# Kernel tuning notes

Hardware: AMD Instinct MI355X
Metric: run time of the kernel (lower is better)

Reference implementation:

```python
import jax, jax.numpy as jnp
import numpy as np

EPS = 1e-7
LN_EPS = 1e-6


def project(x):
    norm = jnp.maximum(jnp.linalg.norm(x, axis=-1, keepdims=True), EPS)
    max_norm = 1.0 - EPS
    return jnp.where(norm >= 1.0, x / norm * max_norm, x)


def mobius_add(x, y, c):
    x2 = jnp.sum(x * x, -1, keepdims=True)
    y2 = jnp.sum(y * y, -1, keepdims=True)
    xy = jnp.sum(x * y, -1, keepdims=True)
    num = (1 + 2 * c * xy + c * y2) * x + (1 - c * x2) * y
    den = 1 + 2 * c * xy + c * c * x2 * y2
    return project(num / jnp.maximum(den, EPS))


def logmap0(y, c):
    sqrt_c = jnp.maximum(jnp.sqrt(c), EPS)
    y_norm = jnp.linalg.norm(y, axis=-1, keepdims=True)
    safe = jnp.maximum(y_norm, EPS)
    mag = jnp.arctanh(jnp.minimum(y_norm, 1.0 - EPS)) / sqrt_c
    return jnp.where(y_norm < EPS, jnp.zeros_like(y), mag * (y / safe))


def expmap0(v, c):
    sqrt_c = jnp.maximum(jnp.sqrt(c), EPS)
    v_norm = jnp.linalg.norm(v, axis=-1, keepdims=True)
    safe = jnp.maximum(v_norm, EPS)
    mag = jnp.tanh(sqrt_c * safe) / sqrt_c
    return project(jnp.where(v_norm < EPS, jnp.zeros_like(v), mag * (v / safe)))


def poincare_dist(x, y, c):
    # x: [B,H,N,1,D], y: [B,H,N,W,D], c: [B,1,1,1,1] -> dist [B,H,N,W]
    sqrt_c = jnp.maximum(jnp.sqrt(c), EPS)
    add_norm = jnp.linalg.norm(mobius_add(-x, y, c), axis=-1)
    arg = jnp.minimum(sqrt_c.squeeze(-1) * add_norm, 1.0 - EPS)
    return 2.0 * jnp.arctanh(arg) / sqrt_c.squeeze(-1)


def sliding_windows(x, window):
    # x: [B,H,N,Dh] -> [B,H,N,window,Dh] of the last `window` keys per query (zero-padded)
    B, H, N, Dh = x.shape
    pad = jnp.zeros((B, H, window - 1, Dh), dtype=x.dtype)
    xp = jnp.concatenate([pad, x], axis=2)
    idx = jnp.arange(window)[None, :] + jnp.arange(N)[:, None]  # [N, W]
    return xp[:, :, idx, :]


def layer_norm(x, scale, bias):
    mu = jnp.mean(x, axis=-1, keepdims=True)
    var = jnp.mean(jnp.square(x - mu), axis=-1, keepdims=True)
    return (x - mu) * jax.lax.rsqrt(var + LN_EPS) * scale + bias


def setup_inputs() -> dict:
    key = jax.random.key(0)
    B, N, DIM, H = 2, 1024, 1024, 16
    Dh = DIM // H
    ks = jax.random.split(key, 16)
    s = 1.0 / np.sqrt(DIM)
    x = 0.01 * jax.random.normal(ks[0], (B, N, DIM), jnp.float32)  # well inside the ball
    # rotary angles: pos * inv_freq, shape [N, Dh//2]
    inv_freq = 1.0 / (10000.0 ** (np.arange(0, Dh // 2, dtype=np.float32) * 2.0 / Dh))
    freqs = jnp.asarray(np.arange(N, dtype=np.float32)[:, None] * inv_freq[None, :])
    c = 0.5 + 0.5 * jax.random.uniform(ks[1], (B,), jnp.float32)
    p = {
        'Wq': s * jax.random.normal(ks[2], (DIM, DIM), jnp.float32), 'bq': jnp.zeros((DIM,), jnp.float32),
        'Wk': s * jax.random.normal(ks[3], (DIM, DIM), jnp.float32), 'bk': jnp.zeros((DIM,), jnp.float32),
        'Wv': s * jax.random.normal(ks[4], (DIM, DIM), jnp.float32), 'bv': jnp.zeros((DIM,), jnp.float32),
        'Wo': s * jax.random.normal(ks[5], (DIM, DIM), jnp.float32), 'bo': jnp.zeros((DIM,), jnp.float32),
        'W1': s * jax.random.normal(ks[6], (DIM, 4 * DIM), jnp.float32), 'b1': jnp.zeros((4 * DIM,), jnp.float32),
        'W2': (1.0 / np.sqrt(4 * DIM)) * jax.random.normal(ks[7], (4 * DIM, DIM), jnp.float32), 'b2': jnp.zeros((DIM,), jnp.float32),
        'ln1_scale': jnp.ones((DIM,), jnp.float32), 'ln1_bias': jnp.zeros((DIM,), jnp.float32),
        'ln2_scale': jnp.ones((DIM,), jnp.float32), 'ln2_bias': jnp.zeros((DIM,), jnp.float32),
        'geo_scale': jnp.ones((H, 1, 1), jnp.float32),
    }
    return dict(x=x, freqs=freqs, c=c, **p)


def reference(x, freqs, c, Wq, bq, Wk, bk, Wv, bv, Wo, bo, W1, b1, W2, b2,
              ln1_scale, ln1_bias, ln2_scale, ln2_bias, geo_scale):
    WINDOW = 32
    B, N, DIM = x.shape
    H = geo_scale.shape[0]
    Dh = DIM // H
    c_ln = c.reshape(B, 1, 1)
    c_attn = c.reshape(B, 1, 1, 1)
    c_d = c.reshape(B, 1, 1, 1, 1)

    # tangent-space layer norm 1
    x_norm = expmap0(layer_norm(logmap0(x, c_ln), ln1_scale, ln1_bias), c_ln)
    x_tan = logmap0(x_norm, c_ln)

    q = (x_tan @ Wq + bq).reshape(B, N, H, Dh)
    k = (x_tan @ Wk + bk).reshape(B, N, H, Dh)
    v = (x_tan @ Wv + bv).reshape(B, N, H, Dh)

    # rotary embedding (real-arithmetic form of complex multiply)
    cos = jnp.cos(freqs).reshape(1, N, 1, Dh // 2)
    sin = jnp.sin(freqs).reshape(1, N, 1, Dh // 2)

    def rope(t):
        t_r, t_i = jnp.split(t, 2, -1)
        return jnp.concatenate([t_r * cos - t_i * sin, t_r * sin + t_i * cos], -1)

    q_hyp = expmap0(rope(q), c_attn)
    k_hyp = expmap0(rope(k), c_attn)

    q_t = q_hyp.transpose(0, 2, 1, 3)  # [B,H,N,Dh]
    k_t = k_hyp.transpose(0, 2, 1, 3)
    v_t = v.transpose(0, 2, 1, 3)

    k_w = sliding_windows(k_t, WINDOW)  # [B,H,N,W,Dh]
    v_w = sliding_windows(v_t, WINDOW)

    dist = poincare_dist(q_t[:, :, :, None, :], k_w, c_d)  # [B,H,N,W]
    attn = jax.nn.softmax(-geo_scale * dist, axis=-1)
    attn_out = jnp.einsum('bhnw,bhnwd->bhnd', attn, v_w).transpose(0, 2, 1, 3).reshape(B, N, DIM)

    attn_hyp = expmap0(attn_out @ Wo + bo, c_ln)
    x_att = mobius_add(x, attn_hyp, c_ln)

    # tangent-space layer norm 2 + hyperbolic FFN
    x_norm2 = expmap0(layer_norm(logmap0(x_att, c_ln), ln2_scale, ln2_bias), c_ln)
    t = logmap0(x_norm2, c_ln)
    ffn_tan = jax.nn.gelu(t @ W1 + b1) @ W2 + b2
    x_ffn = expmap0(ffn_tan, c_ln)
    return mobius_add(x_att, x_ffn, c_ln)
```

## Files before the change

kernel.cpp:

```cpp
#include <hip/hip_runtime.h>
#include <cmath>

static constexpr int SEQ = 1024;
static constexpr int DIM = 1024;
static constexpr int NH  = 16;
static constexpr int DH  = 64;
static constexpr int WB  = 2;
static constexpr int ROWS = WB * SEQ;
__device__ static constexpr double D_EPS = 1e-7;

typedef unsigned short ushort_t;
typedef __attribute__((ext_vector_type(8))) short short8v;
typedef __attribute__((ext_vector_type(4))) float float4v;

__device__ __forceinline__ uint32_t bf16_hi_bits(float f) {
  uint32_t u = __float_as_uint(f);
  return (u + 0x7fffu + ((u >> 16) & 1u)) >> 16;
}

__device__ __forceinline__ size_t tiled_addr(int row, int col, int Kld) {
  return ((size_t)(row >> 7) * (Kld >> 5) + (col >> 5)) * 4096
       + (size_t)((((row >> 4) & 7) << 9) + (((col >> 3) & 3) << 7) + ((row & 15) << 3) + (col & 7));
}
__device__ __forceinline__ void store_hl(ushort_t* __restrict__ hi, ushort_t* __restrict__ lo,
                                         size_t addr, float f) {
  const uint32_t hb = bf16_hi_bits(f);
  hi[addr] = (ushort_t)hb;
  lo[addr] = (ushort_t)bf16_hi_bits(f - __uint_as_float(hb << 16));
}

__device__ __forceinline__ double wsum64(double v) {
#pragma unroll
  for (int m = 32; m >= 1; m >>= 1) v += __shfl_xor(v, m, 64);
  return v;
}

__global__ __launch_bounds__(256) void conv_w_kernel(
    const float* __restrict__ W, ushort_t* __restrict__ hi, ushort_t* __restrict__ lo,
    int K, int N) {
  const int tid = blockIdx.x * 256 + threadIdx.x;
  const int n = tid % N;
  const int k0 = (tid / N) << 3;
  uint32_t hw[4], lw[4];
#pragma unroll
  for (int rp = 0; rp < 4; rp++) {
    uint32_t h2[2], l2[2];
#pragma unroll
    for (int e = 0; e < 2; e++) {
      const float f = W[(size_t)(k0 + rp * 2 + e) * N + n];
      const uint32_t hb = bf16_hi_bits(f);
      h2[e] = hb;
      l2[e] = bf16_hi_bits(f - __uint_as_float(hb << 16));
    }
    hw[rp] = h2[0] | (h2[1] << 16);
    lw[rp] = l2[0] | (l2[1] << 16);
  }
  const size_t addr = tiled_addr(n, k0, K);
  *(uint4*)&hi[addr] = *(uint4*)hw;
  *(uint4*)&lo[addr] = *(uint4*)lw;
}

__global__ __launch_bounds__(256) void ln_tan_kernel(
    const float* __restrict__ xin, const float* __restrict__ cb,
    const float* __restrict__ gamma, const float* __restrict__ beta,
    ushort_t* __restrict__ ohi, ushort_t* __restrict__ olo) {
  __shared__ double sh[2][4];
  const int row = blockIdx.x;
  const int b = row / SEQ;
  const float* xr = xin + (size_t)row * DIM;
  const int t = threadIdx.x;
  float xv[4];
  double s0 = 0.0, s1 = 0.0;
#pragma unroll
  for (int i = 0; i < 4; i++) {
    xv[i] = xr[t + 256 * i];
    s0 += (double)xv[i];
    s1 += (double)xv[i] * (double)xv[i];
  }
  s0 = wsum64(s0); s1 = wsum64(s1);
  const int wid = t >> 6, lane = t & 63;
  if (lane == 0) { sh[0][wid] = s0; sh[1][wid] = s1; }
  __syncthreads();
  s0 = sh[0][0] + sh[0][1] + sh[0][2] + sh[0][3];
  s1 = sh[1][0] + sh[1][1] + sh[1][2] + sh[1][3];

  const double cc  = (double)cb[b];
  const double sqc = fmax(sqrt(cc), D_EPS);
  const double xn  = sqrt(s1);
  double a = 0.0;
  if (xn >= D_EPS) a = atanh(fmin(xn, 1.0 - D_EPS)) / sqc / fmax(xn, D_EPS);
  const double mu   = a * s0 / (double)DIM;
  const double var  = a * a * s1 / (double)DIM - mu * mu;
  const double invs = 1.0 / sqrt(var + 1e-6);

  double tv[4]; double s2 = 0.0;
#pragma unroll
  for (int i = 0; i < 4; i++) {
    const int col = t + 256 * i;
    tv[i] = (a * (double)xv[i] - mu) * invs * (double)gamma[col] + (double)beta[col];
    s2 += tv[i] * tv[i];
  }
  s2 = wsum64(s2);
  __syncthreads();
  if (lane == 0) sh[0][wid] = s2;
  __syncthreads();
  s2 = sh[0][0] + sh[0][1] + sh[0][2] + sh[0][3];

  const double tn = sqrt(s2);
  double C = 0.0;
  if (tn >= D_EPS) {
    const double safe_t = fmax(tn, D_EPS);
    const double mag2 = tanh(sqc * safe_t) / sqc;
    const double en = mag2 * (tn / safe_t);
    const double pn = fmax(en, D_EPS);
    const double f  = (pn >= 1.0) ? (1.0 - D_EPS) / pn : 1.0;
    const double yn = en * f;
    if (yn >= D_EPS) {
      const double mag3 = atanh(fmin(yn, 1.0 - D_EPS)) / sqc;
      C = (mag2 / safe_t) * f * (mag3 / fmax(yn, D_EPS));
    }
  }
#pragma unroll
  for (int i = 0; i < 4; i++) {
    const int col = t + 256 * i;
    store_hl(ohi, olo, tiled_addr(row, col, DIM), (float)(tv[i] * C));
  }
}

__global__ __launch_bounds__(256) void expmobius_parts4_kernel(
    const float* __restrict__ xb,
    const float* __restrict__ p0, const float* __restrict__ p1,
    const float* __restrict__ p2, const float* __restrict__ p3,
    const float* __restrict__ bias, const float* __restrict__ cb,
    float* __restrict__ out) {
  __shared__ double sh[3][4];
  const int row = blockIdx.x;
  const int b = row / SEQ;
  const size_t ro = (size_t)row * DIM;
  const int t = threadIdx.x;
  float xv[4];
  double tv[4];
  double sx2 = 0.0, st2 = 0.0, sxt = 0.0;
#pragma unroll
  for (int i = 0; i < 4; i++) {
    const int col = t + 256 * i;
    xv[i] = xb[ro + col];
    tv[i] = (double)p0[ro + col] + (double)p1[ro + col] +
            (double)p2[ro + col] + (double)p3[ro + col] + (double)bias[col];
    sx2 += (double)xv[i] * (double)xv[i];
    st2 += tv[i] * tv[i];
    sxt += (double)xv[i] * tv[i];
  }
  sx2 = wsum64(sx2); st2 = wsum64(st2); sxt = wsum64(sxt);
  const int wid = t >> 6, lane = t & 63;
  if (lane == 0) { sh[0][wid] = sx2; sh[1][wid] = st2; sh[2][wid] = sxt; }
  __syncthreads();
  sx2 = sh[0][0] + sh[0][1] + sh[0][2] + sh[0][3];
  st2 = sh[1][0] + sh[1][1] + sh[1][2] + sh[1][3];
  sxt = sh[2][0] + sh[2][1] + sh[2][2] + sh[2][3];

  const double cc  = (double)cb[b];
  const double sqc = fmax(sqrt(cc), D_EPS);
  const double tn = sqrt(st2);
  double s = 0.0;
  if (tn >= D_EPS) {
    const double safe = fmax(tn, D_EPS);
    const double mag = tanh(sqc * safe) / sqc;
    const double en = mag * (tn / safe);
    const double pn = fmax(en, D_EPS);
    const double f  = (pn >= 1.0) ? (1.0 - D_EPS) / pn : 1.0;
    s = (mag / safe) * f;
  }
  const double x2 = sx2, y2 = s * s * st2, xy = s * sxt;
  const double P   = 1.0 + 2.0 * cc * xy + cc * y2;
  const double Q   = 1.0 - cc * x2;
  const double den = fmax(1.0 + 2.0 * cc * xy + cc * cc * x2 * y2, D_EPS);
  const double num2 = P * P * x2 + Q * Q * y2 + 2.0 * P * Q * xy;
  const double rn  = sqrt(fmax(num2, 0.0)) / den;
  const double pn2 = fmax(rn, D_EPS);
  const double pf  = (pn2 >= 1.0) ? (1.0 - D_EPS) / pn2 : 1.0;
  const double Pd = (P / den) * pf;
  const double Qd = (Q / den) * pf * s;
#pragma unroll
  for (int i = 0; i < 4; i++)
    out[ro + t + 256 * i] = (float)(Pd * (double)xv[i] + Qd * tv[i]);
}

__global__ __launch_bounds__(256) void rope_expmap_kernel(
    float* __restrict__ q, float* __restrict__ k,
    const float* __restrict__ freqs, const float* __restrict__ cb) {
  const int row = blockIdx.x;
  const int b = row / SEQ, n = row % SEQ;
  const int t = threadIdx.x;
  const int h = t >> 4, j = t & 15;
  const int p1 = j, p2 = j + 16;
  const double f1 = (double)freqs[n * (DH / 2) + p1];
  const double f2 = (double)freqs[n * (DH / 2) + p2];
  const double c1 = cos(f1), s1 = sin(f1);
  const double c2 = cos(f2), s2 = sin(f2);
  const double cc  = (double)cb[b];
  const double sqc = fmax(sqrt(cc), D_EPS);
  const size_t base = (size_t)row * DIM + (size_t)h * DH;
  float* arrs[2] = {q, k};
#pragma unroll
  for (int a = 0; a < 2; a++) {
    float* p = arrs[a] + base;
    const double xr1 = p[p1], xi1 = p[p1 + 32];
    const double xr2 = p[p2], xi2 = p[p2 + 32];
    const double r1 = xr1 * c1 - xi1 * s1, i1 = xr1 * s1 + xi1 * c1;
    const double r2 = xr2 * c2 - xi2 * s2, i2 = xr2 * s2 + xi2 * c2;
    double nrm2 = r1 * r1 + i1 * i1 + r2 * r2 + i2 * i2;
#pragma unroll
    for (int m = 8; m >= 1; m >>= 1) nrm2 += __shfl_xor(nrm2, m, 16);
    const double vn = sqrt(nrm2);
    double sc = 0.0;
    if (vn >= D_EPS) {
      const double safe = fmax(vn, D_EPS);
      const double mag = tanh(sqc * safe) / sqc;
      const double en = mag * (vn / safe);
      const double pn = fmax(en, D_EPS);
      const double f  = (pn >= 1.0) ? (1.0 - D_EPS) / pn : 1.0;
      sc = (mag / safe) * f;
    }
    p[p1] = (float)(r1 * sc); p[p1 + 32] = (float)(i1 * sc);
    p[p2] = (float)(r2 * sc); p[p2 + 32] = (float)(i2 * sc);
  }
}

__global__ __launch_bounds__(256) void attn_kernel(
    const float* __restrict__ qh, const float* __restrict__ kh,
    const float* __restrict__ v, const float* __restrict__ cb,
    const float* __restrict__ geo,
    ushort_t* __restrict__ ohi, ushort_t* __restrict__ olo) {
  __shared__ float qs[8][DH];
  const int g = threadIdx.x >> 5;
  const int w = threadIdx.x & 31;
  const int gid = blockIdx.x * 8 + g;
  const int n = gid & (SEQ - 1);
  const int bh = gid >> 10;
  const int h = bh & (NH - 1);
  const int b = bh >> 4;
  const int row = b * SEQ + n;
  const size_t qbase = (size_t)row * DIM + (size_t)h * DH;
  qs[g][w] = qh[qbase + w];
  qs[g][w + 32] = qh[qbase + w + 32];
  __syncthreads();

  const double cc  = (double)cb[b];
  const double sqc = fmax(sqrt(cc), D_EPS);
  double q2p = (double)qs[g][w] * qs[g][w] + (double)qs[g][w + 32] * qs[g][w + 32];
#pragma unroll
  for (int m = 16; m >= 1; m >>= 1) q2p += __shfl_xor(q2p, m, 32);
  const double a2 = q2p;

  const int msrc = n - 31 + w;
  double y2 = 0.0, qy = 0.0;
  if (msrc >= 0) {
    const float* kr = kh + ((size_t)(b * SEQ + msrc)) * DIM + (size_t)h * DH;
#pragma unroll 8
    for (int d = 0; d < DH; d++) {
      const double kv = (double)kr[d];
      y2 += kv * kv;
      qy += (double)qs[g][d] * kv;
    }
  }
  const double ay = -qy;
  const double P = 1.0 + 2.0 * cc * ay + cc * y2;
  const double Q = 1.0 - cc * a2;
  const double den = fmax(1.0 + 2.0 * cc * ay + cc * cc * a2 * y2, D_EPS);
  const double num2 = P * P * a2 + Q * Q * y2 + 2.0 * P * Q * ay;
  const double rn = sqrt(fmax(num2, 0.0)) / den;
  const double pn = fmax(rn, D_EPS);
  const double addn = (pn >= 1.0) ? (1.0 - D_EPS) * (rn / pn) : rn;
  const double arg = fmin(sqc * addn, 1.0 - D_EPS);
  const double dist = 2.0 * atanh(arg) / sqc;
  const double logit = -(double)geo[h] * dist;

  double mx = logit;
#pragma unroll
  for (int m = 16; m >= 1; m >>= 1) mx = fmax(mx, __shfl_xor(mx, m, 32));
  const double e = exp(logit - mx);
  double se = e;
#pragma unroll
  for (int m = 16; m >= 1; m >>= 1) se += __shfl_xor(se, m, 32);
  const double p = e / se;

  double acc1 = 0.0, acc2 = 0.0;
  for (int wp = 0; wp < 32; wp++) {
    const double pw = __shfl(p, wp, 32);
    const int mp = n - 31 + wp;
    if (mp >= 0) {
      const float* vr = v + ((size_t)(b * SEQ + mp)) * DIM + (size_t)h * DH;
      acc1 += pw * (double)vr[w];
      acc2 += pw * (double)vr[w + 32];
    }
  }
  const int col = h * DH + w;
  store_hl(ohi, olo, tiled_addr(row, col, DIM), (float)acc1);
  store_hl(ohi, olo, tiled_addr(row, col + 32, DIM), (float)acc2);
}

__device__ __forceinline__ float gelu_tanh(float x) {
  const float x3 = x * x * x;
  return 0.5f * x * (1.0f + tanhf(0.7978845608028654f * (x + 0.044715f * x3)));
}

template <int EPI>
__device__ __forceinline__ void mfma_gemm_body(
    const ushort_t* __restrict__ Ahi, const ushort_t* __restrict__ Alo, int Kld,
    const ushort_t* __restrict__ Bhi, const ushort_t* __restrict__ Blo, int KB,
    const float* __restrict__ bias, float* __restrict__ Cf,
    ushort_t* __restrict__ Chi, ushort_t* __restrict__ Clo, int KldOut,
    int N, int k0, int klen, int m0, int n0) {
  __shared__ __align__(16) short AsH[4096], AsL[4096], BsH[4096], BsL[4096];
  const int t = threadIdx.x;
  const int lane = t & 63, wave = t >> 6;
  const int wm = (wave >> 1) << 6, wn = (wave & 1) << 6;
  const size_t abase = (size_t)(m0 >> 7) * (Kld >> 5) * 4096;
  const size_t bbase = (size_t)(n0 >> 7) * (KB >> 5) * 4096;

  float4v acc[4][4];
#pragma unroll
  for (int i = 0; i < 4; i++)
#pragma unroll
    for (int j = 0; j < 4; j++) acc[i][j] = (float4v){0.f, 0.f, 0.f, 0.f};

  uint4 rah0, rah1, ral0, ral1, rbh0, rbh1, rbl0, rbl1;
  {
    const size_t at = abase + (size_t)(k0 >> 5) * 4096;
    const size_t bt = bbase + (size_t)(k0 >> 5) * 4096;
    rah0 = ((const uint4*)(Ahi + at))[t]; rah1 = ((const uint4*)(Ahi + at))[t + 256];
    ral0 = ((const uint4*)(Alo + at))[t]; ral1 = ((const uint4*)(Alo + at))[t + 256];
    rbh0 = ((const uint4*)(Bhi + bt))[t]; rbh1 = ((const uint4*)(Bhi + bt))[t + 256];
    rbl0 = ((const uint4*)(Blo + bt))[t]; rbl1 = ((const uint4*)(Blo + bt))[t + 256];
  }

  for (int kt = 0; kt < klen; kt += 32) {
    __syncthreads();
    ((uint4*)AsH)[t] = rah0; ((uint4*)AsH)[t + 256] = rah1;
    ((uint4*)AsL)[t] = ral0; ((uint4*)AsL)[t + 256] = ral1;
    ((uint4*)BsH)[t] = rbh0; ((uint4*)BsH)[t + 256] = rbh1;
    ((uint4*)BsL)[t] = rbl0; ((uint4*)BsL)[t + 256] = rbl1;
    __syncthreads();
    {
      const int ktn = (kt + 32 < klen) ? kt + 32 : kt;
      const size_t at = abase + (size_t)((k0 + ktn) >> 5) * 4096;
      const size_t bt = bbase + (size_t)((k0 + ktn) >> 5) * 4096;
      rah0 = ((const uint4*)(Ahi + at))[t]; rah1 = ((const uint4*)(Ahi + at))[t + 256];
      ral0 = ((const uint4*)(Alo + at))[t]; ral1 = ((const uint4*)(Alo + at))[t + 256];
      rbh0 = ((const uint4*)(Bhi + bt))[t]; rbh1 = ((const uint4*)(Bhi + bt))[t + 256];
      rbl0 = ((const uint4*)(Blo + bt))[t]; rbl1 = ((const uint4*)(Blo + bt))[t + 256];
    }
    short8v aH[4], aL[4];
    const int ams = wm >> 4;
#pragma unroll
    for (int im = 0; im < 4; im++) {
      aH[im] = *(const short8v*)&AsH[(((ams + im) << 6) + lane) << 3];
      aL[im] = *(const short8v*)&AsL[(((ams + im) << 6) + lane) << 3];
    }
    const int bns = wn >> 4;
#pragma unroll
    for (int in_ = 0; in_ < 4; in_++) {
      const short8v bH = *(const short8v*)&BsH[(((bns + in_) << 6) + lane) << 3];
      const short8v bL = *(const short8v*)&BsL[(((bns + in_) << 6) + lane) << 3];
#pragma unroll
      for (int im = 0; im < 4; im++) {
        acc[im][in_] = __builtin_amdgcn_mfma_f32_16x16x32_bf16(aH[im], bH, acc[im][in_], 0, 0, 0);
        acc[im][in_] = __builtin_amdgcn_mfma_f32_16x16x32_bf16(aH[im], bL, acc[im][in_], 0, 0, 0);
        acc[im][in_] = __builtin_amdgcn_mfma_f32_16x16x32_bf16(aL[im], bH, acc[im][in_], 0, 0, 0);
      }
    }
  }
  const int cq = lane >> 4, ci = lane & 15;
#pragma unroll
  for (int im = 0; im < 4; im++) {
    const int row = m0 + wm + im * 16 + cq * 4;
#pragma unroll
    for (int in_ = 0; in_ < 4; in_++) {
      const int col = n0 + wn + in_ * 16 + ci;
      if (EPI == 2) {
#pragma unroll
        for (int r = 0; r < 4; r++) Cf[(size_t)(row + r) * N + col] = acc[im][in_][r];
      } else if (EPI == 0) {
        const float bv_ = bias[col];
#pragma unroll
        for (int r = 0; r < 4; r++) Cf[(size_t)(row + r) * N + col] = acc[im][in_][r] + bv_;
      } else {
        const float bv_ = bias[col];
#pragma unroll
        for (int r = 0; r < 4; r++)
          store_hl(Chi, Clo, tiled_addr(row + r, col, KldOut),
                   gelu_tanh(acc[im][in_][r] + bv_));
      }
    }
  }
}

__global__ __launch_bounds__(256) void qkv_mfma(
    const ushort_t* __restrict__ Ahi, const ushort_t* __restrict__ Alo,
    const ushort_t* __restrict__ Whi, const ushort_t* __restrict__ Wlo,
    const float* __restrict__ bq, const float* __restrict__ bk, const float* __restrict__ bv,
    float* __restrict__ Cq, float* __restrict__ Ck, float* __restrict__ Cv) {
  const int which = blockIdx.x >> 3;
  const int n0 = (blockIdx.x & 7) << 7;
  const size_t woff = (size_t)which * (1u << 20);
  const float* bias = (which == 0) ? bq : (which == 1) ? bk : bv;
  float* C = (which == 0) ? Cq : (which == 1) ? Ck : Cv;
  mfma_gemm_body<0>(Ahi, Alo, DIM, Whi + woff, Wlo + woff, DIM, bias, C,
                    nullptr, nullptr, 0, DIM, 0, DIM, blockIdx.y << 7, n0);
}

__global__ __launch_bounds__(256) void ffn_up_mfma(
    const ushort_t* __restrict__ Ahi, const ushort_t* __restrict__ Alo,
    const ushort_t* __restrict__ W1hi, const ushort_t* __restrict__ W1lo,
    const float* __restrict__ b1, ushort_t* __restrict__ Hhi, ushort_t* __restrict__ Hlo) {
  mfma_gemm_body<1>(Ahi, Alo, DIM, W1hi, W1lo, DIM, b1, nullptr, Hhi, Hlo, 4 * DIM,
                    4 * DIM, 0, DIM, blockIdx.y << 7, blockIdx.x << 7);
}

__global__ __launch_bounds__(256) void gemm_splitk_mfma(
    const ushort_t* __restrict__ Ahi, const ushort_t* __restrict__ Alo, int Kld,
    const ushort_t* __restrict__ Bhi, const ushort_t* __restrict__ Blo, int KB,
    float* __restrict__ C0, float* __restrict__ C1,
    float* __restrict__ C2, float* __restrict__ C3, int N, int klen) {
  const int z = blockIdx.z;
  float* C = (z == 0) ? C0 : (z == 1) ? C1 : (z == 2) ? C2 : C3;
  mfma_gemm_body<2>(Ahi, Alo, Kld, Bhi, Blo, KB, nullptr, C, nullptr, nullptr, 0,
                    N, z * klen, klen, blockIdx.y << 7, blockIdx.x << 7);
}

extern "C" void kernel_launch(void* const* d_in, const int* in_sizes, int n_in,
                              void* d_out, int out_size, void* d_ws, size_t ws_size,
                              hipStream_t stream) {
  const float* x     = (const float*)d_in[0];
  const float* freqs = (const float*)d_in[1];
  const float* c     = (const float*)d_in[2];
  const float* Wq = (const float*)d_in[3];  const float* bq = (const float*)d_in[4];
  const float* Wk = (const float*)d_in[5];  const float* bk = (const float*)d_in[6];
  const float* Wv = (const float*)d_in[7];  const float* bv = (const float*)d_in[8];
  const float* Wo = (const float*)d_in[9];  const float* bo = (const float*)d_in[10];
  const float* W1 = (const float*)d_in[11]; const float* b1 = (const float*)d_in[12];
  const float* W2 = (const float*)d_in[13]; const float* b2 = (const float*)d_in[14];
  const float* g1 = (const float*)d_in[15]; const float* be1 = (const float*)d_in[16];
  const float* g2 = (const float*)d_in[17]; const float* be2 = (const float*)d_in[18];
  const float* geo = (const float*)d_in[19];
  float* out = (float*)d_out;
  float* ws = (float*)d_ws;

  const size_t SZ = (size_t)ROWS * DIM;
  const size_t PL = SZ;
  const uint32_t M1 = 1u << 20;
  auto us = [&](int i) { return (ushort_t*)(ws + (size_t)i * SZ); };

  ushort_t* xt_hi = us(0);           ushort_t* xt_lo = us(0) + PL;
  float* qb = ws + 1 * SZ; float* kb = ws + 2 * SZ; float* vb = ws + 3 * SZ;
  ushort_t* at_hi = us(4);           ushort_t* at_lo = us(4) + PL;
  ushort_t* qkvo_hi = us(5);         ushort_t* qkvo_lo = us(6);
  ushort_t* w1_hi = us(7);           ushort_t* w1_lo = us(8);
  ushort_t* w2_hi = us(5);           ushort_t* w2_lo = us(6);
  ushort_t* t2_hi = us(4);           ushort_t* t2_lo = us(4) + PL;
  ushort_t* h1_hi = us(0);           ushort_t* h1_lo = us(2);
  float* x_att = out;

  conv_w_kernel<<<512, 256, 0, stream>>>(Wq, qkvo_hi + 0 * M1, qkvo_lo + 0 * M1, DIM, DIM);
  conv_w_kernel<<<512, 256, 0, stream>>>(Wk, qkvo_hi + 1 * M1, qkvo_lo + 1 * M1, DIM, DIM);
  conv_w_kernel<<<512, 256, 0, stream>>>(Wv, qkvo_hi + 2 * M1, qkvo_lo + 2 * M1, DIM, DIM);
  conv_w_kernel<<<512, 256, 0, stream>>>(Wo, qkvo_hi + 3 * M1, qkvo_lo + 3 * M1, DIM, DIM);
  conv_w_kernel<<<2048, 256, 0, stream>>>(W1, w1_hi, w1_lo, DIM, 4 * DIM);
  ln_tan_kernel<<<ROWS, 256, 0, stream>>>(x, c, g1, be1, xt_hi, xt_lo);
  qkv_mfma<<<dim3(24, ROWS / 128), 256, 0, stream>>>(
      xt_hi, xt_lo, qkvo_hi, qkvo_lo, bq, bk, bv, qb, kb, vb);
  rope_expmap_kernel<<<ROWS, 256, 0, stream>>>(qb, kb, freqs, c);
  attn_kernel<<<WB * NH * SEQ / 8, 256, 0, stream>>>(qb, kb, vb, c, geo, at_hi, at_lo);
  gemm_splitk_mfma<<<dim3(DIM / 128, ROWS / 128, 4), 256, 0, stream>>>(
      at_hi, at_lo, DIM, qkvo_hi + 3 * M1, qkvo_lo + 3 * M1, DIM,
      ws + 0 * SZ, ws + 1 * SZ, ws + 2 * SZ, ws + 3 * SZ, DIM, DIM / 4);
  conv_w_kernel<<<2048, 256, 0, stream>>>(W2, w2_hi, w2_lo, 4 * DIM, DIM);
  expmobius_parts4_kernel<<<ROWS, 256, 0, stream>>>(
      x, ws + 0 * SZ, ws + 1 * SZ, ws + 2 * SZ, ws + 3 * SZ, bo, c, x_att);
  ln_tan_kernel<<<ROWS, 256, 0, stream>>>(x_att, c, g2, be2, t2_hi, t2_lo);
  ffn_up_mfma<<<dim3(4 * DIM / 128, ROWS / 128), 256, 0, stream>>>(
      t2_hi, t2_lo, w1_hi, w1_lo, b1, h1_hi, h1_lo);
  gemm_splitk_mfma<<<dim3(DIM / 128, ROWS / 128, 4), 256, 0, stream>>>(
      h1_hi, h1_lo, 4 * DIM, w2_hi, w2_lo, 4 * DIM,
      ws + 4 * SZ, ws + 7 * SZ, ws + 8 * SZ, ws + 9 * SZ, DIM, DIM);
  expmobius_parts4_kernel<<<ROWS, 256, 0, stream>>>(
      x_att, ws + 4 * SZ, ws + 7 * SZ, ws + 8 * SZ, ws + 9 * SZ, b2, c, out);
  (void)in_sizes; (void)n_in; (void)out_size; (void)ws_size;
}
```

Measured before the change: 430.6 us.

## Rework MFMA GEMMs to 32x32x16 tiles with direct global-to-LDS loads

The shared GEMM body now uses 32x32x16 bf16 MFMA instructions with 128-thread blocks, each wave owning a 64x128 output slab. The tiled hi/lo bf16 layout is changed to match the 32x32 operand fragments. Tiles are staged with global_load_lds straight into LDS instead of through registers, which drops the register prefetch and so loses the overlap of the next tile's loads with the current MFMAs. The five weight-conversion launches before the QKV GEMM are merged into one kernel to cut launch overhead.

```diff
diff --git a/kernel.cpp b/kernel.cpp
--- a/kernel.cpp
+++ b/kernel.cpp
@@ -11,7 +11,12 @@
 
 typedef unsigned short ushort_t;
 typedef __attribute__((ext_vector_type(8))) short short8v;
-typedef __attribute__((ext_vector_type(4))) float float4v;
+typedef __attribute__((ext_vector_type(16))) float float16v;
+
+#define GLOAD_LDS(gp, lp)                                                   \
+  __builtin_amdgcn_global_load_lds(                                         \
+      (const __attribute__((address_space(1))) uint32_t*)(gp),              \
+      (__attribute__((address_space(3))) uint32_t*)(lp), 16, 0, 0)
 
 __device__ __forceinline__ uint32_t bf16_hi_bits(float f) {
   uint32_t u = __float_as_uint(f);
@@ -20,7 +25,8 @@
 
 __device__ __forceinline__ size_t tiled_addr(int row, int col, int Kld) {
   return ((size_t)(row >> 7) * (Kld >> 5) + (col >> 5)) * 4096
-       + (size_t)((((row >> 4) & 7) << 9) + (((col >> 3) & 3) << 7) + ((row & 15) << 3) + (col & 7));
+       + (size_t)((((((col >> 4) & 1) << 2) + ((row >> 5) & 3)) << 9)
+       + (((row & 31) | (((col >> 3) & 1) << 5)) << 3) + (col & 7));
 }
 __device__ __forceinline__ void store_hl(ushort_t* __restrict__ hi, ushort_t* __restrict__ lo,
                                          size_t addr, float f) {
@@ -35,10 +41,9 @@
   return v;
 }
 
-__global__ __launch_bounds__(256) void conv_w_kernel(
+__device__ __forceinline__ void conv_w_body(
     const float* __restrict__ W, ushort_t* __restrict__ hi, ushort_t* __restrict__ lo,
-    int K, int N) {
-  const int tid = blockIdx.x * 256 + threadIdx.x;
+    int K, int N, int tid) {
   const int n = tid % N;
   const int k0 = (tid / N) << 3;
   uint32_t hw[4], lw[4];
@@ -58,6 +63,30 @@
   const size_t addr = tiled_addr(n, k0, K);
   *(uint4*)&hi[addr] = *(uint4*)hw;
   *(uint4*)&lo[addr] = *(uint4*)lw;
+}
+
+__global__ __launch_bounds__(256) void conv_all_kernel(
+    const float* __restrict__ Wq, const float* __restrict__ Wk,
+    const float* __restrict__ Wv, const float* __restrict__ Wo,
+    const float* __restrict__ W1,
+    ushort_t* __restrict__ qkvo_hi, ushort_t* __restrict__ qkvo_lo,
+    ushort_t* __restrict__ w1_hi, ushort_t* __restrict__ w1_lo) {
+  const int blk = blockIdx.x;
+  if (blk < 2048) {
+    const int which = blk >> 9;
+    const float* W = (which == 0) ? Wq : (which == 1) ? Wk : (which == 2) ? Wv : Wo;
+    const size_t off = (size_t)which << 20;
+    conv_w_body(W, qkvo_hi + off, qkvo_lo + off, DIM, DIM,
+                (blk & 511) * 256 + threadIdx.x);
+  } else {
+    conv_w_body(W1, w1_hi, w1_lo, DIM, 4 * DIM, (blk - 2048) * 256 + threadIdx.x);
+  }
+}
+
+__global__ __launch_bounds__(256) void conv_w_kernel(
+    const float* __restrict__ W, ushort_t* __restrict__ hi, ushort_t* __restrict__ lo,
+    int K, int N) {
+  conv_w_body(W, hi, lo, K, N, blockIdx.x * 256 + threadIdx.x);
 }
 
 __global__ __launch_bounds__(256) void ln_tan_kernel(
@@ -312,105 +341,95 @@
     const float* __restrict__ bias, float* __restrict__ Cf,
     ushort_t* __restrict__ Chi, ushort_t* __restrict__ Clo, int KldOut,
     int N, int k0, int klen, int m0, int n0) {
-  __shared__ __align__(16) short AsH[4096], AsL[4096], BsH[4096], BsL[4096];
+  __shared__ __align__(16) ushort_t AsH[4096], AsL[4096], BsH[4096], BsL[4096];
   const int t = threadIdx.x;
   const int lane = t & 63, wave = t >> 6;
-  const int wm = (wave >> 1) << 6, wn = (wave & 1) << 6;
   const size_t abase = (size_t)(m0 >> 7) * (Kld >> 5) * 4096;
   const size_t bbase = (size_t)(n0 >> 7) * (KB >> 5) * 4096;
 
-  float4v acc[4][4];
-#pragma unroll
-  for (int i = 0; i < 4; i++)
-#pragma unroll
-    for (int j = 0; j < 4; j++) acc[i][j] = (float4v){0.f, 0.f, 0.f, 0.f};
-
-  uint4 rah0, rah1, ral0, ral1, rbh0, rbh1, rbl0, rbl1;
-  {
-    const size_t at = abase + (size_t)(k0 >> 5) * 4096;
-    const size_t bt = bbase + (size_t)(k0 >> 5) * 4096;
-    rah0 = ((const uint4*)(Ahi + at))[t]; rah1 = ((const uint4*)(Ahi + at))[t + 256];
-    ral0 = ((const uint4*)(Alo + at))[t]; ral1 = ((const uint4*)(Alo + at))[t + 256];
-    rbh0 = ((const uint4*)(Bhi + bt))[t]; rbh1 = ((const uint4*)(Bhi + bt))[t + 256];
-    rbl0 = ((const uint4*)(Blo + bt))[t]; rbl1 = ((const uint4*)(Blo + bt))[t + 256];
-  }
+  float16v acc[2][4];
+#pragma unroll
+  for (int i = 0; i < 2; i++)
+#pragma unroll
+    for (int j = 0; j < 4; j++)
+#pragma unroll
+      for (int r = 0; r < 16; r++) acc[i][j][r] = 0.f;
 
   for (int kt = 0; kt < klen; kt += 32) {
+    const size_t at = abase + (size_t)((k0 + kt) >> 5) * 4096;
+    const size_t bt = bbase + (size_t)((k0 + kt) >> 5) * 4096;
     __syncthreads();
-    ((uint4*)AsH)[t] = rah0; ((uint4*)AsH)[t + 256] = rah1;
-    ((uint4*)AsL)[t] = ral0; ((uint4*)AsL)[t + 256] = ral1;
-    ((uint4*)BsH)[t] = rbh0; ((uint4*)BsH)[t + 256] = rbh1;
-    ((uint4*)BsL)[t] = rbl0; ((uint4*)BsL)[t + 256] = rbl1;
+#pragma unroll
+    for (int c = 0; c < 4; c++) {
+      const int go = (c << 10) + (t << 3);
+      const int lo = (c << 10) + (wave << 9);
+      GLOAD_LDS(Ahi + at + go, AsH + lo);
+      GLOAD_LDS(Alo + at + go, AsL + lo);
+      GLOAD_LDS(Bhi + bt + go, BsH + lo);
+      GLOAD_LDS(Blo + bt + go, BsL + lo);
+    }
     __syncthreads();
-    {
-      const int ktn = (kt + 32 < klen) ? kt + 32 : kt;
-      const size_t at = abase + (size_t)((k0 + ktn) >> 5) * 4096;
-      const size_t bt = bbase + (size_t)((k0 + ktn) >> 5) * 4096;
-      rah0 = ((const uint4*)(Ahi + at))[t]; rah1 = ((const uint4*)(Ahi + at))[t + 256];
-      ral0 = ((const uint4*)(Alo + at))[t]; ral1 = ((const uint4*)(Alo + at))[t + 256];
-      rbh0 = ((const uint4*)(Bhi + bt))[t]; rbh1 = ((const uint4*)(Bhi + bt))[t + 256];
-      rbl0 = ((const uint4*)(Blo + bt))[t]; rbl1 = ((const uint4*)(Blo + bt))[t + 256];
-    }
-    short8v aH[4], aL[4];
-    const int ams = wm >> 4;
-#pragma unroll
-    for (int im = 0; im < 4; im++) {
-      aH[im] = *(const short8v*)&AsH[(((ams + im) << 6) + lane) << 3];
-      aL[im] = *(const short8v*)&AsL[(((ams + im) << 6) + lane) << 3];
-    }
-    const int bns = wn >> 4;
-#pragma unroll
-    for (int in_ = 0; in_ < 4; in_++) {
-      const short8v bH = *(const short8v*)&BsH[(((bns + in_) << 6) + lane) << 3];
-      const short8v bL = *(const short8v*)&BsL[(((bns + in_) << 6) + lane) << 3];
-#pragma unroll
-      for (int im = 0; im < 4; im++) {
-        acc[im][in_] = __builtin_amdgcn_mfma_f32_16x16x32_bf16(aH[im], bH, acc[im][in_], 0, 0, 0);
-        acc[im][in_] = __builtin_amdgcn_mfma_f32_16x16x32_bf16(aH[im], bL, acc[im][in_], 0, 0, 0);
-        acc[im][in_] = __builtin_amdgcn_mfma_f32_16x16x32_bf16(aL[im], bH, acc[im][in_], 0, 0, 0);
+#pragma unroll
+    for (int ks = 0; ks < 2; ks++) {
+      short8v aH[2], aL[2];
+#pragma unroll
+      for (int im = 0; im < 2; im++) {
+        const int ms = (wave << 1) + im;
+        const int off = (((ks << 2) + ms) << 9) + (lane << 3);
+        aH[im] = *(const short8v*)&AsH[off];
+        aL[im] = *(const short8v*)&AsL[off];
       }
-    }
-  }
-  const int cq = lane >> 4, ci = lane & 15;
-#pragma unroll
-  for (int im = 0; im < 4; im++) {
-    const int row = m0 + wm + im * 16 + cq * 4;
-#pragma unroll
-    for (int in_ = 0; in_ < 4; in_++) {
-      const int col = n0 + wn + in_ * 16 + ci;
-      if (EPI == 2) {
-#pragma unroll
-        for (int r = 0; r < 4; r++) Cf[(size_t)(row + r) * N + col] = acc[im][in_][r];
-      } else if (EPI == 0) {
-        const float bv_ = bias[col];
-#pragma unroll
-        for (int r = 0; r < 4; r++) Cf[(size_t)(row + r) * N + col] = acc[im][in_][r] + bv_;
-      } else {
-        const float bv_ = bias[col];
-#pragma unroll
-        for (int r = 0; r < 4; r++)
-          store_hl(Chi, Clo, tiled_addr(row + r, col, KldOut),
-                   gelu_tanh(acc[im][in_][r] + bv_));
+#pragma unroll
+      for (int ns = 0; ns < 4; ns++) {
+        const int off = (((ks << 2) + ns) << 9) + (lane << 3);
+        const short8v bH = *(const short8v*)&BsH[off];
+        const short8v bL = *(const short8v*)&BsL[off];
+#pragma unroll
+        for (int im = 0; im < 2; im++) {
+          acc[im][ns] = __builtin_amdgcn_mfma_f32_32x32x16_bf16(aH[im], bH, acc[im][ns], 0, 0, 0);
+          acc[im][ns] = __builtin_amdgcn_mfma_f32_32x32x16_bf16(aH[im], bL, acc[im][ns], 0, 0, 0);
+          acc[im][ns] = __builtin_amdgcn_mfma_f32_32x32x16_bf16(aL[im], bH, acc[im][ns], 0, 0, 0);
+        }
       }
     }
   }
-}
-
-__global__ __launch_bounds__(256) void qkv_mfma(
+  const int cn = lane & 31, ch = lane >> 5;
+#pragma unroll
+  for (int im = 0; im < 2; im++) {
+    const int rbase = m0 + (wave << 6) + (im << 5) + (ch << 2);
+#pragma unroll
+    for (int ns = 0; ns < 4; ns++) {
+      const int col = n0 + (ns << 5) + cn;
+      const float bv_ = (EPI == 2) ? 0.f : bias[col];
+#pragma unroll
+      for (int r = 0; r < 16; r++) {
+        const int row = rbase + (r & 3) + ((r >> 2) << 3);
+        const float val = acc[im][ns][r] + bv_;
+        if (EPI == 1) {
+          store_hl(Chi, Clo, tiled_addr(row, col, KldOut), gelu_tanh(val));
+        } else {
+          Cf[(size_t)row * N + col] = val;
+        }
+      }
+    }
+  }
+}
+
+__global__ __launch_bounds__(128, 2) void qkv_mfma(
     const ushort_t* __restrict__ Ahi, const ushort_t* __restrict__ Alo,
     const ushort_t* __restrict__ Whi, const ushort_t* __restrict__ Wlo,
     const float* __restrict__ bq, const float* __restrict__ bk, const float* __restrict__ bv,
     float* __restrict__ Cq, float* __restrict__ Ck, float* __restrict__ Cv) {
   const int which = blockIdx.x >> 3;
   const int n0 = (blockIdx.x & 7) << 7;
-  const size_t woff = (size_t)which * (1u << 20);
+  const size_t woff = (size_t)which << 20;
   const float* bias = (which == 0) ? bq : (which == 1) ? bk : bv;
   float* C = (which == 0) ? Cq : (which == 1) ? Ck : Cv;
   mfma_gemm_body<0>(Ahi, Alo, DIM, Whi + woff, Wlo + woff, DIM, bias, C,
                     nullptr, nullptr, 0, DIM, 0, DIM, blockIdx.y << 7, n0);
 }
 
-__global__ __launch_bounds__(256) void ffn_up_mfma(
+__global__ __launch_bounds__(128, 2) void ffn_up_mfma(
     const ushort_t* __restrict__ Ahi, const ushort_t* __restrict__ Alo,
     const ushort_t* __restrict__ W1hi, const ushort_t* __restrict__ W1lo,
     const float* __restrict__ b1, ushort_t* __restrict__ Hhi, ushort_t* __restrict__ Hlo) {
@@ -418,7 +437,7 @@
                     4 * DIM, 0, DIM, blockIdx.y << 7, blockIdx.x << 7);
 }
 
-__global__ __launch_bounds__(256) void gemm_splitk_mfma(
+__global__ __launch_bounds__(128, 2) void gemm_splitk_mfma(
     const ushort_t* __restrict__ Ahi, const ushort_t* __restrict__ Alo, int Kld,
     const ushort_t* __restrict__ Bhi, const ushort_t* __restrict__ Blo, int KB,
     float* __restrict__ C0, float* __restrict__ C1,
@@ -462,26 +481,23 @@
   ushort_t* h1_hi = us(0);           ushort_t* h1_lo = us(2);
   float* x_att = out;
 
-  conv_w_kernel<<<512, 256, 0, stream>>>(Wq, qkvo_hi + 0 * M1, qkvo_lo + 0 * M1, DIM, DIM);
-  conv_w_kernel<<<512, 256, 0, stream>>>(Wk, qkvo_hi + 1 * M1, qkvo_lo + 1 * M1, DIM, DIM);
-  conv_w_kernel<<<512, 256, 0, stream>>>(Wv, qkvo_hi + 2 * M1, qkvo_lo + 2 * M1, DIM, DIM);
-  conv_w_kernel<<<512, 256, 0, stream>>>(Wo, qkvo_hi + 3 * M1, qkvo_lo + 3 * M1, DIM, DIM);
-  conv_w_kernel<<<2048, 256, 0, stream>>>(W1, w1_hi, w1_lo, DIM, 4 * DIM);
+  conv_all_kernel<<<4096, 256, 0, stream>>>(
+      Wq, Wk, Wv, Wo, W1, qkvo_hi, qkvo_lo, w1_hi, w1_lo);
   ln_tan_kernel<<<ROWS, 256, 0, stream>>>(x, c, g1, be1, xt_hi, xt_lo);
-  qkv_mfma<<<dim3(24, ROWS / 128), 256, 0, stream>>>(
+  qkv_mfma<<<dim3(24, ROWS / 128), 128, 0, stream>>>(
       xt_hi, xt_lo, qkvo_hi, qkvo_lo, bq, bk, bv, qb, kb, vb);
   rope_expmap_kernel<<<ROWS, 256, 0, stream>>>(qb, kb, freqs, c);
   attn_kernel<<<WB * NH * SEQ / 8, 256, 0, stream>>>(qb, kb, vb, c, geo, at_hi, at_lo);
-  gemm_splitk_mfma<<<dim3(DIM / 128, ROWS / 128, 4), 256, 0, stream>>>(
+  gemm_splitk_mfma<<<dim3(DIM / 128, ROWS / 128, 4), 128, 0, stream>>>(
       at_hi, at_lo, DIM, qkvo_hi + 3 * M1, qkvo_lo + 3 * M1, DIM,
       ws + 0 * SZ, ws + 1 * SZ, ws + 2 * SZ, ws + 3 * SZ, DIM, DIM / 4);
   conv_w_kernel<<<2048, 256, 0, stream>>>(W2, w2_hi, w2_lo, 4 * DIM, DIM);
   expmobius_parts4_kernel<<<ROWS, 256, 0, stream>>>(
       x, ws + 0 * SZ, ws + 1 * SZ, ws + 2 * SZ, ws + 3 * SZ, bo, c, x_att);
   ln_tan_kernel<<<ROWS, 256, 0, stream>>>(x_att, c, g2, be2, t2_hi, t2_lo);
-  ffn_up_mfma<<<dim3(4 * DIM / 128, ROWS / 128), 256, 0, stream>>>(
+  ffn_up_mfma<<<dim3(4 * DIM / 128, ROWS / 128), 128, 0, stream>>>(
       t2_hi, t2_lo, w1_hi, w1_lo, b1, h1_hi, h1_lo);
-  gemm_splitk_mfma<<<dim3(DIM / 128, ROWS / 128, 4), 256, 0, stream>>>(
+  gemm_splitk_mfma<<<dim3(DIM / 128, ROWS / 128, 4), 128, 0, stream>>>(
       h1_hi, h1_lo, 4 * DIM, w2_hi, w2_lo, 4 * DIM,
       ws + 4 * SZ, ws + 7 * SZ, ws + 8 * SZ, ws + 9 * SZ, DIM, DIM);
   expmobius_parts4_kernel<<<ROWS, 256, 0, stream>>>(
```

New measurement: 498.1 us. 1.16x slower.
